# Kernel tuning notes

Hardware: AMD Instinct MI355X
Metric: run time of the kernel (lower is better)

Reference implementation:

```python
import jax, jax.numpy as jnp
import numpy as np

D_MODEL, N_HEADS, D_VALUE = 512, 8, 64
D_HEAD = D_MODEL // N_HEADS


def setup_inputs() -> dict:
    key = jax.random.key(0)
    ks = jax.random.split(key, 5)
    B, T = 2, 2048
    x = jax.random.normal(ks[0], (B, T, D_MODEL), dtype=jnp.float32)
    # torch nn.Linear convention: W has shape [out_features, in_features]
    scale = 0.02
    W_q = jax.random.normal(ks[1], (N_HEADS * D_HEAD, D_MODEL), dtype=jnp.float32) * scale
    W_k = jax.random.normal(ks[2], (N_HEADS * D_HEAD, D_MODEL), dtype=jnp.float32) * scale
    W_v = jax.random.normal(ks[3], (N_HEADS * D_VALUE, D_MODEL), dtype=jnp.float32) * scale
    W_out = jax.random.normal(ks[4], (D_MODEL, N_HEADS * D_VALUE), dtype=jnp.float32) * scale
    return {"x": x, "W_q": W_q, "W_k": W_k, "W_v": W_v, "W_out": W_out}


def _elu_feature_map(t):
    # phi(t) = elu(t) + 1
    return jax.nn.elu(t) + 1.0


def reference(x, W_q, W_k, W_v, W_out):
    B, T, D = x.shape
    H, dh, dv = N_HEADS, D_HEAD, D_VALUE
    # projections (Linear without bias: x @ W.T)
    Q = _elu_feature_map((x @ W_q.T).reshape(B, T, H, dh)).transpose(0, 2, 1, 3)  # [B,H,T,dh]
    K = _elu_feature_map((x @ W_k.T).reshape(B, T, H, dh)).transpose(0, 2, 1, 3)  # [B,H,T,dh]
    V = (x @ W_v.T).reshape(B, T, H, dv).transpose(0, 2, 1, 3)                    # [B,H,T,dv]
    # causal linear attention via cumulative outer-product state
    KV = jnp.einsum('bhti,bhtj->bhtij', K, V)       # [B,H,T,dh,dv]
    S = jnp.cumsum(KV, axis=2)                      # running state
    z = jnp.cumsum(K, axis=2)                       # running normalizer
    num = jnp.einsum('bhti,bhtij->bhtj', Q, S)      # [B,H,T,dv]
    den = jnp.maximum(jnp.einsum('bhti,bhti->bht', Q, z), 1e-6)[..., None]
    out = (num / den).transpose(0, 2, 1, 3).reshape(B, T, H * dv)
    return out @ W_out.T
```

## Files before the change

### kernel.cpp

```cpp
#include <hip/hip_runtime.h>
#include <hip/hip_bf16.h>

#define T_SEQ 2048
#define BATCH 2
#define DMODEL 512
#define NHEAD 8
#define DHEAD 64
#define DVAL 64
#define BH 16
#define CHUNK 64
#define NCHUNK 32
#define MROWS 4096

typedef __bf16 bf16;
typedef __bf16 bf16x8 __attribute__((ext_vector_type(8)));
typedef __bf16 bf16x4 __attribute__((ext_vector_type(4)));
typedef float f32x4 __attribute__((ext_vector_type(4)));

__device__ inline void gload_lds16(const bf16* g, bf16* l) {
  __builtin_amdgcn_global_load_lds((const __attribute__((address_space(1))) void*)g,
                                   (__attribute__((address_space(3))) void*)l, 16, 0, 0);
}

__device__ inline int sw_t(int row, int g) {
  return ((g ^ (row & 7) ^ (row >> 3)) << 3);
}

__global__ __launch_bounds__(256) void k_convert(const float* __restrict__ x,
                          const float* __restrict__ wq,
                          const float* __restrict__ wk,
                          const float* __restrict__ wv,
                          const float* __restrict__ wo,
                          bf16* __restrict__ x_bf,
                          bf16* __restrict__ wqkv_bf,
                          bf16* __restrict__ wo_bf) {
  const int W = DMODEL * DMODEL;
  int i = blockIdx.x * 256 + threadIdx.x;
  {
    f32x4 v = ((const f32x4*)x)[i];
    bf16x4 o; o[0] = (bf16)v[0]; o[1] = (bf16)v[1]; o[2] = (bf16)v[2]; o[3] = (bf16)v[3];
    *(bf16x4*)(x_bf + (size_t)i * 4) = o;
  }
  if (i < W / 4) {
    f32x4 a = ((const f32x4*)wq)[i];
    f32x4 b = ((const f32x4*)wk)[i];
    f32x4 c = ((const f32x4*)wv)[i];
    f32x4 d = ((const f32x4*)wo)[i];
    bf16x4 oa, ob, oc, od;
#pragma unroll
    for (int u = 0; u < 4; u++) { oa[u] = (bf16)a[u]; ob[u] = (bf16)b[u]; oc[u] = (bf16)c[u]; od[u] = (bf16)d[u]; }
    *(bf16x4*)(wqkv_bf + (size_t)i * 4) = oa;
    *(bf16x4*)(wqkv_bf + W + (size_t)i * 4) = ob;
    *(bf16x4*)(wqkv_bf + 2 * W + (size_t)i * 4) = oc;
    *(bf16x4*)(wo_bf + (size_t)i * 4) = od;
  }
}

__global__ __launch_bounds__(256) void k_gemm_qkv(const bf16* __restrict__ A,
                                                  const bf16* __restrict__ B,
                                                  bf16* __restrict__ Q,
                                                  bf16* __restrict__ K,
                                                  bf16* __restrict__ V) {
  __shared__ bf16 sh[12288];
  bf16* As = sh;
  bf16* Bs = sh + 4096;
  const int tid = threadIdx.x;
  const int wvi = tid >> 6, lane = tid & 63;
  const int c = lane & 15, quad = lane >> 4;
  const int m_tile = blockIdx.x * 64, n_tile = blockIdx.y * 128;
  const int r8 = lane >> 3, gp = lane & 7;
  const bf16* Abase = A + (size_t)m_tile * DMODEL;
  const bf16* Bbase = B + (size_t)n_tile * DMODEL;
  const int wn = wvi * 32;

  f32x4 acc[4][2] = {};

  for (int k0 = 0; k0 < DMODEL; k0 += 64) {
    if (k0) __syncthreads();
#pragma unroll
    for (int r = 0; r < 2; r++) {
      int t8 = wvi * 2 + r;
      const bf16* ga = Abase + (size_t)(t8 * 8 + r8) * DMODEL + k0 + ((gp ^ r8) << 3);
      gload_lds16(ga, As + t8 * 8 * 64);
    }
#pragma unroll
    for (int r = 0; r < 4; r++) {
      int t8 = wvi * 4 + r;
      const bf16* gb = Bbase + (size_t)(t8 * 8 + r8) * DMODEL + k0 + ((gp ^ r8) << 3);
      gload_lds16(gb, Bs + t8 * 8 * 64);
    }
    __syncthreads();
#pragma unroll
    for (int ks = 0; ks < 2; ks++) {
      bf16x8 af[4], bfr[2];
#pragma unroll
      for (int i = 0; i < 4; i++)
        af[i] = *(const bf16x8*)(As + (i * 16 + c) * 64 + (((ks * 4 + quad) ^ (c & 7)) << 3));
#pragma unroll
      for (int j = 0; j < 2; j++)
        bfr[j] = *(const bf16x8*)(Bs + (wn + j * 16 + c) * 64 + (((ks * 4 + quad) ^ (c & 7)) << 3));
#pragma unroll
      for (int i = 0; i < 4; i++)
#pragma unroll
        for (int j = 0; j < 2; j++)
          acc[i][j] = __builtin_amdgcn_mfma_f32_16x16x32_bf16(af[i], bfr[j], acc[i][j], 0, 0, 0);
    }
  }

  const bool is_qk = (n_tile < 1024);
  __syncthreads();
#pragma unroll
  for (int i = 0; i < 4; i++)
#pragma unroll
    for (int j = 0; j < 2; j++)
#pragma unroll
      for (int r = 0; r < 4; r++) {
        int row = i * 16 + quad * 4 + r;
        int col = wn + j * 16 + c;
        float v = acc[i][j][r];
        if (is_qk) v = (v > 0.f) ? (v + 1.f) : __expf(v);
        sh[row * 132 + col] = (bf16)v;
      }
  __syncthreads();
  bf16* dst = (n_tile < 512) ? Q : ((n_tile < 1024) ? K : V);
  int nb = n_tile & 511;
#pragma unroll
  for (int q = 0; q < 4; q++) {
    int row = q * 16 + (tid >> 4);
    int col0 = (tid & 15) * 8;
    bf16x8 v8 = *(const bf16x8*)(sh + row * 132 + col0);
    *(bf16x8*)(dst + (size_t)(m_tile + row) * 512 + nb + col0) = v8;
  }
}

__global__ __launch_bounds__(256) void k_gemm_out(const bf16* __restrict__ A,
                                                  const bf16* __restrict__ B,
                                                  float* __restrict__ out) {
  __shared__ bf16 sh[8192];
  bf16* As = sh;
  bf16* Bs = sh + 4096;
  const int tid = threadIdx.x;
  const int wvi = tid >> 6, lane = tid & 63;
  const int c = lane & 15, quad = lane >> 4;
  const int m_tile = blockIdx.x * 64, n_tile = blockIdx.y * 64;
  const int r8 = lane >> 3, gp = lane & 7;
  const bf16* Abase = A + (size_t)m_tile * DMODEL;
  const bf16* Bbase = B + (size_t)n_tile * DMODEL;
  const int wn = wvi * 16;

  f32x4 acc[4] = {};

  for (int k0 = 0; k0 < DMODEL; k0 += 64) {
    if (k0) __syncthreads();
#pragma unroll
    for (int r = 0; r < 2; r++) {
      int t8 = wvi * 2 + r;
      const bf16* ga = Abase + (size_t)(t8 * 8 + r8) * DMODEL + k0 + ((gp ^ r8) << 3);
      gload_lds16(ga, As + t8 * 8 * 64);
    }
#pragma unroll
    for (int r = 0; r < 2; r++) {
      int t8 = wvi * 2 + r;
      const bf16* gb = Bbase + (size_t)(t8 * 8 + r8) * DMODEL + k0 + ((gp ^ r8) << 3);
      gload_lds16(gb, Bs + t8 * 8 * 64);
    }
    __syncthreads();
#pragma unroll
    for (int ks = 0; ks < 2; ks++) {
      bf16x8 af[4], bfr;
#pragma unroll
      for (int i = 0; i < 4; i++)
        af[i] = *(const bf16x8*)(As + (i * 16 + c) * 64 + (((ks * 4 + quad) ^ (c & 7)) << 3));
      bfr = *(const bf16x8*)(Bs + (wn + c) * 64 + (((ks * 4 + quad) ^ (c & 7)) << 3));
#pragma unroll
      for (int i = 0; i < 4; i++)
        acc[i] = __builtin_amdgcn_mfma_f32_16x16x32_bf16(af[i], bfr, acc[i], 0, 0, 0);
    }
  }

  float* shf = (float*)sh;
#pragma unroll
  for (int p = 0; p < 2; p++) {
    __syncthreads();
#pragma unroll
    for (int i2 = 0; i2 < 2; i2++) {
      int i = 2 * p + i2;
#pragma unroll
      for (int r = 0; r < 4; r++)
        shf[(i2 * 16 + quad * 4 + r) * 68 + wn + c] = acc[i][r];
    }
    __syncthreads();
    int row = tid >> 3, col0 = (tid & 7) * 8;
#pragma unroll
    for (int q4 = 0; q4 < 2; q4++) {
      f32x4 v4 = *(const f32x4*)(shf + row * 68 + col0 + q4 * 4);
      *(f32x4*)(out + (size_t)(m_tile + p * 32 + row) * 512 + n_tile + col0 + q4 * 4) = v4;
    }
  }
}

__global__ __launch_bounds__(256) void k_state(const bf16* __restrict__ K,
                                               const bf16* __restrict__ V,
                                               bf16* __restrict__ KVs,
                                               float* __restrict__ zsum) {
  __shared__ bf16 Kt[4096];
  __shared__ bf16 Vt[4096];
  int chunk = blockIdx.x, bh = blockIdx.y;
  int b = bh >> 3, h = bh & 7;
  int tid = threadIdx.x, lane = tid & 63, wvi = tid >> 6;
  int rowbase = b * T_SEQ + chunk * CHUNK;

#pragma unroll
  for (int p = 0; p < 2; p++) {
    int r = p * 32 + (tid >> 3);
    int j0 = (tid & 7) * 8;
    bf16x8 kk  = *(const bf16x8*)(K + (size_t)(rowbase + r) * 512 + h * 64 + j0);
    bf16x8 vvv = *(const bf16x8*)(V + (size_t)(rowbase + r) * 512 + h * 64 + j0);
#pragma unroll
    for (int u = 0; u < 8; u++) {
      int row = j0 + u;
      Kt[row * 64 + sw_t(row, r >> 3) + (r & 7)] = kk[u];
      Vt[row * 64 + sw_t(row, r >> 3) + (r & 7)] = vvv[u];
    }
  }
  __syncthreads();

  int c = lane & 15, quad = lane >> 4;
  f32x4 acc[4] = {};
#pragma unroll
  for (int ks = 0; ks < 2; ks++) {
    int ar = wvi * 16 + c;
    bf16x8 a = *(const bf16x8*)(Vt + ar * 64 + sw_t(ar, ks * 4 + quad));
#pragma unroll
    for (int f = 0; f < 4; f++) {
      int br = f * 16 + c;
      bf16x8 bb = *(const bf16x8*)(Kt + br * 64 + sw_t(br, ks * 4 + quad));
      acc[f] = __builtin_amdgcn_mfma_f32_16x16x32_bf16(a, bb, acc[f], 0, 0, 0);
    }
  }
  bf16* op = KVs + ((size_t)(bh * NCHUNK + chunk) << 12);
  bf16x8 lo, hi;
#pragma unroll
  for (int u = 0; u < 8; u++) {
    lo[u] = (bf16)acc[u >> 2][u & 3];
    hi[u] = (bf16)acc[2 + (u >> 2)][u & 3];
  }
  *(bf16x8*)(op + tid * 16) = lo;
  *(bf16x8*)(op + tid * 16 + 8) = hi;

  if (tid < 64) {
    float s = 0.f;
#pragma unroll
    for (int g = 0; g < 8; g++) {
      bf16x8 kr = *(const bf16x8*)(Kt + tid * 64 + sw_t(tid, g));
#pragma unroll
      for (int u = 0; u < 8; u++) s += (float)kr[u];
    }
    zsum[(size_t)(bh * NCHUNK + chunk) * 64 + tid] = s;
  }
}

__global__ __launch_bounds__(256) void k_attn(const bf16* __restrict__ Q,
                                              const bf16* __restrict__ K,
                                              const bf16* __restrict__ V,
                                              const bf16* __restrict__ KVs,
                                              const float* __restrict__ zsum,
                                              bf16* __restrict__ O) {
  __shared__ bf16 SH[20480];
  bf16* Qs   = SH;
  bf16* Ks   = SH + 4096;
  bf16* Vt   = SH + 8192;
  bf16* Asm  = SH + 12288;
  bf16* Spre = SH + 16384;
  __shared__ float zp4[4][64];
  __shared__ float zpre[64], rsum[64], den[64];

  int chunk = blockIdx.x, bh = blockIdx.y;
  int b = bh >> 3, h = bh & 7;
  int tid = threadIdx.x, lane = tid & 63, wvi = tid >> 6;
  int c = lane & 15, quad = lane >> 4;
  int rowbase = b * T_SEQ + chunk * CHUNK;

#pragma unroll
  for (int p = 0; p < 2; p++) {
    int rbase = p * 32 + wvi * 8;
    int r8 = lane >> 3, gp = lane & 7;
    const bf16* gq = Q + (size_t)(rowbase + rbase + r8) * 512 + h * 64 + ((gp ^ r8) << 3);
    const bf16* gk = K + (size_t)(rowbase + rbase + r8) * 512 + h * 64 + ((gp ^ r8) << 3);
    gload_lds16(gq, Qs + rbase * 64);
    gload_lds16(gk, Ks + rbase * 64);
  }

#pragma unroll
  for (int p = 0; p < 2; p++) {
    int r = p * 32 + (tid >> 3);
    int j0 = (tid & 7) * 8;
    bf16x8 vvv = *(const bf16x8*)(V + (size_t)(rowbase + r) * 512 + h * 64 + j0);
#pragma unroll
    for (int u = 0; u < 8; u++) {
      int row = j0 + u;
      Vt[row * 64 + sw_t(row, r >> 3) + (r & 7)] = vvv[u];
    }
  }

  {
    float accp[16];
#pragma unroll
    for (int u = 0; u < 16; u++) accp[u] = 0.f;
    const bf16* base = KVs + ((size_t)(bh * NCHUNK) << 12) + tid * 16;
    for (int cc = 0; cc < chunk; cc++) {
      const bf16* pp = base + ((size_t)cc << 12);
      bf16x8 a0 = *(const bf16x8*)pp;
      bf16x8 a1 = *(const bf16x8*)(pp + 8);
#pragma unroll
      for (int u = 0; u < 8; u++) { accp[u] += (float)a0[u]; accp[8 + u] += (float)a1[u]; }
    }
#pragma unroll
    for (int s = 0; s < 16; s++) {
      int rowp = wvi * 16 + quad * 4 + (s & 3);
      int colp = (s >> 2) * 16 + c;
      Spre[rowp * 64 + sw_t(rowp, colp >> 3) + (colp & 7)] = (bf16)accp[s];
    }
  }
  {
    int i = tid & 63, qq = tid >> 6;
    float s = 0.f;
    for (int cc = qq; cc < chunk; cc += 4)
      s += zsum[(size_t)(bh * NCHUNK + cc) * 64 + i];
    zp4[qq][i] = s;
  }
  __syncthreads();
  if (tid < 64) zpre[tid] = zp4[0][tid] + zp4[1][tid] + zp4[2][tid] + zp4[3][tid];

  f32x4 sacc[4] = {};
#pragma unroll
  for (int ks = 0; ks < 2; ks++) {
    int ar = 16 * wvi + c;
    bf16x8 a = *(const bf16x8*)(Qs + ar * 64 + (((ks * 4 + quad) ^ (c & 7)) << 3));
#pragma unroll
    for (int j = 0; j < 4; j++) {
      int br = 16 * j + c;
      bf16x8 bb = *(const bf16x8*)(Ks + br * 64 + (((ks * 4 + quad) ^ (c & 7)) << 3));
      sacc[j] = __builtin_amdgcn_mfma_f32_16x16x32_bf16(a, bb, sacc[j], 0, 0, 0);
    }
  }

  float rs[4] = {0.f, 0.f, 0.f, 0.f};
#pragma unroll
  for (int j = 0; j < 4; j++) {
#pragma unroll
    for (int r = 0; r < 4; r++) {
      int t = 16 * wvi + quad * 4 + r, s = 16 * j + c;
      float v = (s <= t) ? sacc[j][r] : 0.f;
      rs[r] += v;
      Asm[t * 64 + sw_t(t, s >> 3) + (s & 7)] = (bf16)v;
    }
  }
#pragma unroll
  for (int r = 0; r < 4; r++) {
    float v = rs[r];
    v += __shfl_xor(v, 1); v += __shfl_xor(v, 2);
    v += __shfl_xor(v, 4); v += __shfl_xor(v, 8);
    if (c == 0) rsum[16 * wvi + quad * 4 + r] = v;
  }
  __syncthreads();

  if (tid < 64) {
    float s = rsum[tid];
    int t7 = tid & 7;
#pragma unroll
    for (int kg = 0; kg < 8; kg++) {
      bf16x8 qv = *(const bf16x8*)(Qs + tid * 64 + ((kg ^ t7) << 3));
#pragma unroll
      for (int u = 0; u < 8; u++) s += (float)qv[u] * zpre[kg * 8 + u];
    }
    den[tid] = fmaxf(s, 1e-6f);
  }

  f32x4 oacc[4] = {};
#pragma unroll
  for (int ks = 0; ks < 2; ks++) {
    int ar = 16 * wvi + c;
    bf16x8 aq = *(const bf16x8*)(Qs + ar * 64 + (((ks * 4 + quad) ^ (c & 7)) << 3));
    bf16x8 aa = *(const bf16x8*)(Asm + ar * 64 + sw_t(ar, ks * 4 + quad));
#pragma unroll
    for (int j = 0; j < 4; j++) {
      int br = 16 * j + c;
      bf16x8 bs = *(const bf16x8*)(Spre + br * 64 + sw_t(br, ks * 4 + quad));
      bf16x8 bv = *(const bf16x8*)(Vt + br * 64 + sw_t(br, ks * 4 + quad));
      oacc[j] = __builtin_amdgcn_mfma_f32_16x16x32_bf16(aq, bs, oacc[j], 0, 0, 0);
      oacc[j] = __builtin_amdgcn_mfma_f32_16x16x32_bf16(aa, bv, oacc[j], 0, 0, 0);
    }
  }
  __syncthreads();

  {
    bf16* shr = SH;
#pragma unroll
    for (int r = 0; r < 4; r++) {
      int t = 16 * wvi + quad * 4 + r;
      float rd = 1.f / den[t];
#pragma unroll
      for (int j = 0; j < 4; j++)
        shr[t * 76 + 16 * j + c] = (bf16)(oacc[j][r] * rd);
    }
    __syncthreads();
    int row = tid >> 2, col0 = (tid & 3) * 16;
    bf16x8 v0 = *(const bf16x8*)(shr + row * 76 + col0);
    bf16x8 v1 = *(const bf16x8*)(shr + row * 76 + col0 + 8);
    bf16* od = O + (size_t)(rowbase + row) * 512 + h * 64 + col0;
    *(bf16x8*)od = v0;
    *(bf16x8*)(od + 8) = v1;
  }
}

extern "C" void kernel_launch(void* const* d_in, const int* in_sizes, int n_in,
                              void* d_out, int out_size, void* d_ws, size_t ws_size,
                              hipStream_t stream) {
  const float* x  = (const float*)d_in[0];
  const float* wq = (const float*)d_in[1];
  const float* wk = (const float*)d_in[2];
  const float* wv = (const float*)d_in[3];
  const float* wo = (const float*)d_in[4];
  float* out = (float*)d_out;

  char* p = (char*)d_ws;
  bf16* x_bf   = (bf16*)p; p += (size_t)MROWS * DMODEL * 2;
  bf16* wqkv_b = (bf16*)p; p += (size_t)3 * DMODEL * DMODEL * 2;
  bf16* wo_b   = (bf16*)p; p += (size_t)DMODEL * DMODEL * 2;
  bf16* Qb     = (bf16*)p; p += (size_t)MROWS * 512 * 2;
  bf16* Kb     = (bf16*)p; p += (size_t)MROWS * 512 * 2;
  bf16* Vb     = (bf16*)p; p += (size_t)MROWS * 512 * 2;
  bf16* Ob     = (bf16*)p; p += (size_t)MROWS * 512 * 2;
  bf16* KVs    = (bf16*)p; p += (size_t)BH * NCHUNK * DHEAD * DVAL * 2;
  float* zs    = (float*)p; p += (size_t)BH * NCHUNK * DHEAD * 4;

  k_convert<<<2048, 256, 0, stream>>>(x, wq, wk, wv, wo, x_bf, wqkv_b, wo_b);
  k_gemm_qkv<<<dim3(MROWS / 64, (3 * DMODEL) / 128), 256, 0, stream>>>(
      x_bf, wqkv_b, Qb, Kb, Vb);
  k_state<<<dim3(NCHUNK, BH), 256, 0, stream>>>(Kb, Vb, KVs, zs);
  k_attn<<<dim3(NCHUNK, BH), 256, 0, stream>>>(Qb, Kb, Vb, KVs, zs, Ob);
  k_gemm_out<<<dim3(MROWS / 64, DMODEL / 64), 256, 0, stream>>>(Ob, wo_b, out);
}
```

Before: 109.9 us.

## Fuse all five stages into one cooperative persistent kernel with grid syncs

Replaces the five separate launches (convert, QKV GEMM, chunk state, attention, output GEMM) with a single cooperative kernel of 768 blocks that separates the stages with grid.sync(). The aim is to remove per-launch overhead and the gaps between kernels on a small problem. In exchange, the grid is capped at 768 resident blocks, later stages leave some blocks idle, and grid-wide barriers have their own cost. Occupancy depends on three blocks fitting per CU with a 42KB shared buffer.

```diff
diff --git a/kernel.cpp b/kernel.cpp
--- a/kernel.cpp
+++ b/kernel.cpp
@@ -1,5 +1,8 @@
 #include <hip/hip_runtime.h>
 #include <hip/hip_bf16.h>
+#include <hip/hip_cooperative_groups.h>
+
+namespace cg = cooperative_groups;
 
 #define T_SEQ 2048
 #define BATCH 2
@@ -12,6 +15,8 @@
 #define NCHUNK 32
 #define MROWS 4096
 
+#define GRID_BLOCKS 768
+
 typedef __bf16 bf16;
 typedef __bf16 bf16x8 __attribute__((ext_vector_type(8)));
 typedef __bf16 bf16x4 __attribute__((ext_vector_type(4)));
@@ -26,391 +31,389 @@
   return ((g ^ (row & 7) ^ (row >> 3)) << 3);
 }
 
-__global__ __launch_bounds__(256) void k_convert(const float* __restrict__ x,
-                          const float* __restrict__ wq,
-                          const float* __restrict__ wk,
-                          const float* __restrict__ wv,
-                          const float* __restrict__ wo,
-                          bf16* __restrict__ x_bf,
-                          bf16* __restrict__ wqkv_bf,
-                          bf16* __restrict__ wo_bf) {
-  const int W = DMODEL * DMODEL;
-  int i = blockIdx.x * 256 + threadIdx.x;
-  {
-    f32x4 v = ((const f32x4*)x)[i];
-    bf16x4 o; o[0] = (bf16)v[0]; o[1] = (bf16)v[1]; o[2] = (bf16)v[2]; o[3] = (bf16)v[3];
-    *(bf16x4*)(x_bf + (size_t)i * 4) = o;
-  }
-  if (i < W / 4) {
-    f32x4 a = ((const f32x4*)wq)[i];
-    f32x4 b = ((const f32x4*)wk)[i];
-    f32x4 c = ((const f32x4*)wv)[i];
-    f32x4 d = ((const f32x4*)wo)[i];
-    bf16x4 oa, ob, oc, od;
-#pragma unroll
-    for (int u = 0; u < 4; u++) { oa[u] = (bf16)a[u]; ob[u] = (bf16)b[u]; oc[u] = (bf16)c[u]; od[u] = (bf16)d[u]; }
-    *(bf16x4*)(wqkv_bf + (size_t)i * 4) = oa;
-    *(bf16x4*)(wqkv_bf + W + (size_t)i * 4) = ob;
-    *(bf16x4*)(wqkv_bf + 2 * W + (size_t)i * 4) = oc;
-    *(bf16x4*)(wo_bf + (size_t)i * 4) = od;
-  }
-}
-
-__global__ __launch_bounds__(256) void k_gemm_qkv(const bf16* __restrict__ A,
-                                                  const bf16* __restrict__ B,
-                                                  bf16* __restrict__ Q,
-                                                  bf16* __restrict__ K,
-                                                  bf16* __restrict__ V) {
-  __shared__ bf16 sh[12288];
-  bf16* As = sh;
-  bf16* Bs = sh + 4096;
+__global__ __launch_bounds__(256, 3) void k_fused(
+    const float* __restrict__ x,
+    const float* __restrict__ wq,
+    const float* __restrict__ wk,
+    const float* __restrict__ wv,
+    const float* __restrict__ wo,
+    bf16* __restrict__ x_bf,
+    bf16* __restrict__ wqkv_bf,
+    bf16* __restrict__ wo_bf,
+    bf16* __restrict__ Qb,
+    bf16* __restrict__ Kb,
+    bf16* __restrict__ Vb,
+    bf16* __restrict__ Ob,
+    bf16* __restrict__ KVs,
+    float* __restrict__ zsum,
+    float* __restrict__ out) {
+  __shared__ __align__(16) char SHB[43008];
+  bf16* sh = (bf16*)SHB;
+
   const int tid = threadIdx.x;
+  const int bid = blockIdx.x;
+  cg::grid_group grid = cg::this_grid();
+
   const int wvi = tid >> 6, lane = tid & 63;
   const int c = lane & 15, quad = lane >> 4;
-  const int m_tile = blockIdx.x * 64, n_tile = blockIdx.y * 128;
   const int r8 = lane >> 3, gp = lane & 7;
-  const bf16* Abase = A + (size_t)m_tile * DMODEL;
-  const bf16* Bbase = B + (size_t)n_tile * DMODEL;
-  const int wn = wvi * 32;
-
-  f32x4 acc[4][2] = {};
-
-  for (int k0 = 0; k0 < DMODEL; k0 += 64) {
-    if (k0) __syncthreads();
-#pragma unroll
-    for (int r = 0; r < 2; r++) {
-      int t8 = wvi * 2 + r;
-      const bf16* ga = Abase + (size_t)(t8 * 8 + r8) * DMODEL + k0 + ((gp ^ r8) << 3);
-      gload_lds16(ga, As + t8 * 8 * 64);
+
+  {
+    const int W = DMODEL * DMODEL;
+    for (int i = bid * 256 + tid; i < (MROWS * DMODEL) / 4; i += GRID_BLOCKS * 256) {
+      f32x4 v = ((const f32x4*)x)[i];
+      bf16x4 o; o[0] = (bf16)v[0]; o[1] = (bf16)v[1]; o[2] = (bf16)v[2]; o[3] = (bf16)v[3];
+      *(bf16x4*)(x_bf + (size_t)i * 4) = o;
+      if (i < W / 4) {
+        f32x4 a = ((const f32x4*)wq)[i];
+        f32x4 b = ((const f32x4*)wk)[i];
+        f32x4 cc = ((const f32x4*)wv)[i];
+        f32x4 d = ((const f32x4*)wo)[i];
+        bf16x4 oa, ob, oc, od;
+#pragma unroll
+        for (int u = 0; u < 4; u++) { oa[u] = (bf16)a[u]; ob[u] = (bf16)b[u]; oc[u] = (bf16)cc[u]; od[u] = (bf16)d[u]; }
+        *(bf16x4*)(wqkv_bf + (size_t)i * 4) = oa;
+        *(bf16x4*)(wqkv_bf + W + (size_t)i * 4) = ob;
+        *(bf16x4*)(wqkv_bf + 2 * W + (size_t)i * 4) = oc;
+        *(bf16x4*)(wo_bf + (size_t)i * 4) = od;
+      }
+    }
+  }
+  grid.sync();
+
+  {
+    bf16* As = sh;
+    bf16* Bs = sh + 4096;
+    const int bx = bid & 63, by = bid >> 6;
+    const int m_tile = bx * 64, n_tile = by * 128;
+    const bf16* Abase = x_bf + (size_t)m_tile * DMODEL;
+    const bf16* Bbase = wqkv_bf + (size_t)n_tile * DMODEL;
+    const int wn = wvi * 32;
+
+    f32x4 acc[4][2] = {};
+
+    for (int k0 = 0; k0 < DMODEL; k0 += 64) {
+      if (k0) __syncthreads();
+#pragma unroll
+      for (int r = 0; r < 2; r++) {
+        int t8 = wvi * 2 + r;
+        const bf16* ga = Abase + (size_t)(t8 * 8 + r8) * DMODEL + k0 + ((gp ^ r8) << 3);
+        gload_lds16(ga, As + t8 * 8 * 64);
+      }
+#pragma unroll
+      for (int r = 0; r < 4; r++) {
+        int t8 = wvi * 4 + r;
+        const bf16* gb = Bbase + (size_t)(t8 * 8 + r8) * DMODEL + k0 + ((gp ^ r8) << 3);
+        gload_lds16(gb, Bs + t8 * 8 * 64);
+      }
+      __syncthreads();
+#pragma unroll
+      for (int ks = 0; ks < 2; ks++) {
+        bf16x8 af[4], bfr[2];
+#pragma unroll
+        for (int i = 0; i < 4; i++)
+          af[i] = *(const bf16x8*)(As + (i * 16 + c) * 64 + (((ks * 4 + quad) ^ (c & 7)) << 3));
+#pragma unroll
+        for (int j = 0; j < 2; j++)
+          bfr[j] = *(const bf16x8*)(Bs + (wn + j * 16 + c) * 64 + (((ks * 4 + quad) ^ (c & 7)) << 3));
+#pragma unroll
+        for (int i = 0; i < 4; i++)
+#pragma unroll
+          for (int j = 0; j < 2; j++)
+            acc[i][j] = __builtin_amdgcn_mfma_f32_16x16x32_bf16(af[i], bfr[j], acc[i][j], 0, 0, 0);
+      }
+    }
+
+    const bool is_qk = (n_tile < 1024);
+    __syncthreads();
+#pragma unroll
+    for (int i = 0; i < 4; i++)
+#pragma unroll
+      for (int j = 0; j < 2; j++)
+#pragma unroll
+        for (int r = 0; r < 4; r++) {
+          int row = i * 16 + quad * 4 + r;
+          int col = wn + j * 16 + c;
+          float v = acc[i][j][r];
+          if (is_qk) v = (v > 0.f) ? (v + 1.f) : __expf(v);
+          sh[row * 132 + col] = (bf16)v;
+        }
+    __syncthreads();
+    bf16* dst = (n_tile < 512) ? Qb : ((n_tile < 1024) ? Kb : Vb);
+    int nb = n_tile & 511;
+#pragma unroll
+    for (int q = 0; q < 4; q++) {
+      int row = q * 16 + (tid >> 4);
+      int col0 = (tid & 15) * 8;
+      bf16x8 v8 = *(const bf16x8*)(sh + row * 132 + col0);
+      *(bf16x8*)(dst + (size_t)(m_tile + row) * 512 + nb + col0) = v8;
+    }
+  }
+  grid.sync();
+
+  if (bid < NCHUNK * BH) {
+    bf16* Kt = sh;
+    bf16* Vt = sh + 4096;
+    int chunk = bid & 31, bh = bid >> 5;
+    int b = bh >> 3, h = bh & 7;
+    int rowbase = b * T_SEQ + chunk * CHUNK;
+
+#pragma unroll
+    for (int p = 0; p < 2; p++) {
+      int r = p * 32 + (tid >> 3);
+      int j0 = (tid & 7) * 8;
+      bf16x8 kk  = *(const bf16x8*)(Kb + (size_t)(rowbase + r) * 512 + h * 64 + j0);
+      bf16x8 vvv = *(const bf16x8*)(Vb + (size_t)(rowbase + r) * 512 + h * 64 + j0);
+#pragma unroll
+      for (int u = 0; u < 8; u++) {
+        int row = j0 + u;
+        Kt[row * 64 + sw_t(row, r >> 3) + (r & 7)] = kk[u];
+        Vt[row * 64 + sw_t(row, r >> 3) + (r & 7)] = vvv[u];
+      }
+    }
+    __syncthreads();
+
+    f32x4 acc[4] = {};
+#pragma unroll
+    for (int ks = 0; ks < 2; ks++) {
+      int ar = wvi * 16 + c;
+      bf16x8 a = *(const bf16x8*)(Vt + ar * 64 + sw_t(ar, ks * 4 + quad));
+#pragma unroll
+      for (int f = 0; f < 4; f++) {
+        int br = f * 16 + c;
+        bf16x8 bb = *(const bf16x8*)(Kt + br * 64 + sw_t(br, ks * 4 + quad));
+        acc[f] = __builtin_amdgcn_mfma_f32_16x16x32_bf16(a, bb, acc[f], 0, 0, 0);
+      }
+    }
+    bf16* op = KVs + ((size_t)(bh * NCHUNK + chunk) << 12);
+    bf16x8 lo, hi;
+#pragma unroll
+    for (int u = 0; u < 8; u++) {
+      lo[u] = (bf16)acc[u >> 2][u & 3];
+      hi[u] = (bf16)acc[2 + (u >> 2)][u & 3];
+    }
+    *(bf16x8*)(op + tid * 16) = lo;
+    *(bf16x8*)(op + tid * 16 + 8) = hi;
+
+    if (tid < 64) {
+      float s = 0.f;
+#pragma unroll
+      for (int g = 0; g < 8; g++) {
+        bf16x8 kr = *(const bf16x8*)(Kt + tid * 64 + sw_t(tid, g));
+#pragma unroll
+        for (int u = 0; u < 8; u++) s += (float)kr[u];
+      }
+      zsum[(size_t)(bh * NCHUNK + chunk) * 64 + tid] = s;
+    }
+  }
+  grid.sync();
+
+  if (bid < NCHUNK * BH) {
+    bf16* Qs   = sh;
+    bf16* Ks   = sh + 4096;
+    bf16* Vt   = sh + 8192;
+    bf16* Asm  = sh + 12288;
+    bf16* Spre = sh + 16384;
+    float* zp4  = (float*)(SHB + 40960);
+    float* zpre = (float*)(SHB + 40960 + 1024);
+    float* rsum = zpre + 64;
+    float* den  = rsum + 64;
+
+    int chunk = bid & 31, bh = bid >> 5;
+    int b = bh >> 3, h = bh & 7;
+    int rowbase = b * T_SEQ + chunk * CHUNK;
+
+#pragma unroll
+    for (int p = 0; p < 2; p++) {
+      int rbase = p * 32 + wvi * 8;
+      const bf16* gq = Qb + (size_t)(rowbase + rbase + r8) * 512 + h * 64 + ((gp ^ r8) << 3);
+      const bf16* gk = Kb + (size_t)(rowbase + rbase + r8) * 512 + h * 64 + ((gp ^ r8) << 3);
+      gload_lds16(gq, Qs + rbase * 64);
+      gload_lds16(gk, Ks + rbase * 64);
+    }
+
+#pragma unroll
+    for (int p = 0; p < 2; p++) {
+      int r = p * 32 + (tid >> 3);
+      int j0 = (tid & 7) * 8;
+      bf16x8 vvv = *(const bf16x8*)(Vb + (size_t)(rowbase + r) * 512 + h * 64 + j0);
+#pragma unroll
+      for (int u = 0; u < 8; u++) {
+        int row = j0 + u;
+        Vt[row * 64 + sw_t(row, r >> 3) + (r & 7)] = vvv[u];
+      }
+    }
+
+    {
+      float accp[16];
+#pragma unroll
+      for (int u = 0; u < 16; u++) accp[u] = 0.f;
+      const bf16* base = KVs + ((size_t)(bh * NCHUNK) << 12) + tid * 16;
+      for (int cc = 0; cc < chunk; cc++) {
+        const bf16* pp = base + ((size_t)cc << 12);
+        bf16x8 a0 = *(const bf16x8*)pp;
+        bf16x8 a1 = *(const bf16x8*)(pp + 8);
+#pragma unroll
+        for (int u = 0; u < 8; u++) { accp[u] += (float)a0[u]; accp[8 + u] += (float)a1[u]; }
+      }
+#pragma unroll
+      for (int s = 0; s < 16; s++) {
+        int rowp = wvi * 16 + quad * 4 + (s & 3);
+        int colp = (s >> 2) * 16 + c;
+        Spre[rowp * 64 + sw_t(rowp, colp >> 3) + (colp & 7)] = (bf16)accp[s];
+      }
+    }
+    {
+      int i = tid & 63, qq = tid >> 6;
+      float s = 0.f;
+      for (int cc = qq; cc < chunk; cc += 4)
+        s += zsum[(size_t)(bh * NCHUNK + cc) * 64 + i];
+      zp4[qq * 64 + i] = s;
+    }
+    __syncthreads();
+    if (tid < 64) zpre[tid] = zp4[0 * 64 + tid] + zp4[1 * 64 + tid] + zp4[2 * 64 + tid] + zp4[3 * 64 + tid];
+
+    f32x4 sacc[4] = {};
+#pragma unroll
+    for (int ks = 0; ks < 2; ks++) {
+      int ar = 16 * wvi + c;
+      bf16x8 a = *(const bf16x8*)(Qs + ar * 64 + (((ks * 4 + quad) ^ (c & 7)) << 3));
+#pragma unroll
+      for (int j = 0; j < 4; j++) {
+        int br = 16 * j + c;
+        bf16x8 bb = *(const bf16x8*)(Ks + br * 64 + (((ks * 4 + quad) ^ (c & 7)) << 3));
+        sacc[j] = __builtin_amdgcn_mfma_f32_16x16x32_bf16(a, bb, sacc[j], 0, 0, 0);
+      }
+    }
+
+    float rs[4] = {0.f, 0.f, 0.f, 0.f};
+#pragma unroll
+    for (int j = 0; j < 4; j++) {
+#pragma unroll
+      for (int r = 0; r < 4; r++) {
+        int t = 16 * wvi + quad * 4 + r, s = 16 * j + c;
+        float v = (s <= t) ? sacc[j][r] : 0.f;
+        rs[r] += v;
+        Asm[t * 64 + sw_t(t, s >> 3) + (s & 7)] = (bf16)v;
+      }
     }
 #pragma unroll
     for (int r = 0; r < 4; r++) {
-      int t8 = wvi * 4 + r;
-      const bf16* gb = Bbase + (size_t)(t8 * 8 + r8) * DMODEL + k0 + ((gp ^ r8) << 3);
-      gload_lds16(gb, Bs + t8 * 8 * 64);
-    }
-    __syncthreads();
+      float v = rs[r];
+      v += __shfl_xor(v, 1); v += __shfl_xor(v, 2);
+      v += __shfl_xor(v, 4); v += __shfl_xor(v, 8);
+      if (c == 0) rsum[16 * wvi + quad * 4 + r] = v;
+    }
+    __syncthreads();
+
+    if (tid < 64) {
+      float s = rsum[tid];
+      int t7 = tid & 7;
+#pragma unroll
+      for (int kg = 0; kg < 8; kg++) {
+        bf16x8 qv = *(const bf16x8*)(Qs + tid * 64 + ((kg ^ t7) << 3));
+#pragma unroll
+        for (int u = 0; u < 8; u++) s += (float)qv[u] * zpre[kg * 8 + u];
+      }
+      den[tid] = fmaxf(s, 1e-6f);
+    }
+
+    f32x4 oacc[4] = {};
 #pragma unroll
     for (int ks = 0; ks < 2; ks++) {
-      bf16x8 af[4], bfr[2];
-#pragma unroll
-      for (int i = 0; i < 4; i++)
-        af[i] = *(const bf16x8*)(As + (i * 16 + c) * 64 + (((ks * 4 + quad) ^ (c & 7)) << 3));
-#pragma unroll
-      for (int j = 0; j < 2; j++)
-        bfr[j] = *(const bf16x8*)(Bs + (wn + j * 16 + c) * 64 + (((ks * 4 + quad) ^ (c & 7)) << 3));
-#pragma unroll
-      for (int i = 0; i < 4; i++)
-#pragma unroll
-        for (int j = 0; j < 2; j++)
-          acc[i][j] = __builtin_amdgcn_mfma_f32_16x16x32_bf16(af[i], bfr[j], acc[i][j], 0, 0, 0);
+      int ar = 16 * wvi + c;
+      bf16x8 aq = *(const bf16x8*)(Qs + ar * 64 + (((ks * 4 + quad) ^ (c & 7)) << 3));
+      bf16x8 aa = *(const bf16x8*)(Asm + ar * 64 + sw_t(ar, ks * 4 + quad));
+#pragma unroll
+      for (int j = 0; j < 4; j++) {
+        int br = 16 * j + c;
+        bf16x8 bs = *(const bf16x8*)(Spre + br * 64 + sw_t(br, ks * 4 + quad));
+        bf16x8 bv = *(const bf16x8*)(Vt + br * 64 + sw_t(br, ks * 4 + quad));
+        oacc[j] = __builtin_amdgcn_mfma_f32_16x16x32_bf16(aq, bs, oacc[j], 0, 0, 0);
+        oacc[j] = __builtin_amdgcn_mfma_f32_16x16x32_bf16(aa, bv, oacc[j], 0, 0, 0);
+      }
+    }
+    __syncthreads();
+
+    {
+      bf16* shr = sh;
+#pragma unroll
+      for (int r = 0; r < 4; r++) {
+        int t = 16 * wvi + quad * 4 + r;
+        float rd = 1.f / den[t];
+#pragma unroll
+        for (int j = 0; j < 4; j++)
+          shr[t * 76 + 16 * j + c] = (bf16)(oacc[j][r] * rd);
+      }
+      __syncthreads();
+      int row = tid >> 2, col0 = (tid & 3) * 16;
+      bf16x8 v0 = *(const bf16x8*)(shr + row * 76 + col0);
+      bf16x8 v1 = *(const bf16x8*)(shr + row * 76 + col0 + 8);
+      bf16* od = Ob + (size_t)(rowbase + row) * 512 + h * 64 + col0;
+      *(bf16x8*)od = v0;
+      *(bf16x8*)(od + 8) = v1;
     }
   }
-
-  const bool is_qk = (n_tile < 1024);
-  __syncthreads();
-#pragma unroll
-  for (int i = 0; i < 4; i++)
-#pragma unroll
-    for (int j = 0; j < 2; j++)
-#pragma unroll
-      for (int r = 0; r < 4; r++) {
-        int row = i * 16 + quad * 4 + r;
-        int col = wn + j * 16 + c;
-        float v = acc[i][j][r];
-        if (is_qk) v = (v > 0.f) ? (v + 1.f) : __expf(v);
-        sh[row * 132 + col] = (bf16)v;
-      }
-  __syncthreads();
-  bf16* dst = (n_tile < 512) ? Q : ((n_tile < 1024) ? K : V);
-  int nb = n_tile & 511;
-#pragma unroll
-  for (int q = 0; q < 4; q++) {
-    int row = q * 16 + (tid >> 4);
-    int col0 = (tid & 15) * 8;
-    bf16x8 v8 = *(const bf16x8*)(sh + row * 132 + col0);
-    *(bf16x8*)(dst + (size_t)(m_tile + row) * 512 + nb + col0) = v8;
-  }
-}
-
-__global__ __launch_bounds__(256) void k_gemm_out(const bf16* __restrict__ A,
-                                                  const bf16* __restrict__ B,
-                                                  float* __restrict__ out) {
-  __shared__ bf16 sh[8192];
-  bf16* As = sh;
-  bf16* Bs = sh + 4096;
-  const int tid = threadIdx.x;
-  const int wvi = tid >> 6, lane = tid & 63;
-  const int c = lane & 15, quad = lane >> 4;
-  const int m_tile = blockIdx.x * 64, n_tile = blockIdx.y * 64;
-  const int r8 = lane >> 3, gp = lane & 7;
-  const bf16* Abase = A + (size_t)m_tile * DMODEL;
-  const bf16* Bbase = B + (size_t)n_tile * DMODEL;
-  const int wn = wvi * 16;
-
-  f32x4 acc[4] = {};
-
-  for (int k0 = 0; k0 < DMODEL; k0 += 64) {
-    if (k0) __syncthreads();
-#pragma unroll
-    for (int r = 0; r < 2; r++) {
-      int t8 = wvi * 2 + r;
-      const bf16* ga = Abase + (size_t)(t8 * 8 + r8) * DMODEL + k0 + ((gp ^ r8) << 3);
-      gload_lds16(ga, As + t8 * 8 * 64);
-    }
-#pragma unroll
-    for (int r = 0; r < 2; r++) {
-      int t8 = wvi * 2 + r;
-      const bf16* gb = Bbase + (size_t)(t8 * 8 + r8) * DMODEL + k0 + ((gp ^ r8) << 3);
-      gload_lds16(gb, Bs + t8 * 8 * 64);
-    }
-    __syncthreads();
-#pragma unroll
-    for (int ks = 0; ks < 2; ks++) {
-      bf16x8 af[4], bfr;
-#pragma unroll
-      for (int i = 0; i < 4; i++)
-        af[i] = *(const bf16x8*)(As + (i * 16 + c) * 64 + (((ks * 4 + quad) ^ (c & 7)) << 3));
-      bfr = *(const bf16x8*)(Bs + (wn + c) * 64 + (((ks * 4 + quad) ^ (c & 7)) << 3));
-#pragma unroll
-      for (int i = 0; i < 4; i++)
-        acc[i] = __builtin_amdgcn_mfma_f32_16x16x32_bf16(af[i], bfr, acc[i], 0, 0, 0);
-    }
-  }
-
-  float* shf = (float*)sh;
-#pragma unroll
-  for (int p = 0; p < 2; p++) {
-    __syncthreads();
-#pragma unroll
-    for (int i2 = 0; i2 < 2; i2++) {
-      int i = 2 * p + i2;
-#pragma unroll
-      for (int r = 0; r < 4; r++)
-        shf[(i2 * 16 + quad * 4 + r) * 68 + wn + c] = acc[i][r];
-    }
-    __syncthreads();
-    int row = tid >> 3, col0 = (tid & 7) * 8;
-#pragma unroll
-    for (int q4 = 0; q4 < 2; q4++) {
-      f32x4 v4 = *(const f32x4*)(shf + row * 68 + col0 + q4 * 4);
-      *(f32x4*)(out + (size_t)(m_tile + p * 32 + row) * 512 + n_tile + col0 + q4 * 4) = v4;
-    }
-  }
-}
-
-__global__ __launch_bounds__(256) void k_state(const bf16* __restrict__ K,
-                                               const bf16* __restrict__ V,
-                                               bf16* __restrict__ KVs,
-                                               float* __restrict__ zsum) {
-  __shared__ bf16 Kt[4096];
-  __shared__ bf16 Vt[4096];
-  int chunk = blockIdx.x, bh = blockIdx.y;
-  int b = bh >> 3, h = bh & 7;
-  int tid = threadIdx.x, lane = tid & 63, wvi = tid >> 6;
-  int rowbase = b * T_SEQ + chunk * CHUNK;
-
-#pragma unroll
-  for (int p = 0; p < 2; p++) {
-    int r = p * 32 + (tid >> 3);
-    int j0 = (tid & 7) * 8;
-    bf16x8 kk  = *(const bf16x8*)(K + (size_t)(rowbase + r) * 512 + h * 64 + j0);
-    bf16x8 vvv = *(const bf16x8*)(V + (size_t)(rowbase + r) * 512 + h * 64 + j0);
-#pragma unroll
-    for (int u = 0; u < 8; u++) {
-      int row = j0 + u;
-      Kt[row * 64 + sw_t(row, r >> 3) + (r & 7)] = kk[u];
-      Vt[row * 64 + sw_t(row, r >> 3) + (r & 7)] = vvv[u];
-    }
-  }
-  __syncthreads();
-
-  int c = lane & 15, quad = lane >> 4;
-  f32x4 acc[4] = {};
-#pragma unroll
-  for (int ks = 0; ks < 2; ks++) {
-    int ar = wvi * 16 + c;
-    bf16x8 a = *(const bf16x8*)(Vt + ar * 64 + sw_t(ar, ks * 4 + quad));
-#pragma unroll
-    for (int f = 0; f < 4; f++) {
-      int br = f * 16 + c;
-      bf16x8 bb = *(const bf16x8*)(Kt + br * 64 + sw_t(br, ks * 4 + quad));
-      acc[f] = __builtin_amdgcn_mfma_f32_16x16x32_bf16(a, bb, acc[f], 0, 0, 0);
-    }
-  }
-  bf16* op = KVs + ((size_t)(bh * NCHUNK + chunk) << 12);
-  bf16x8 lo, hi;
-#pragma unroll
-  for (int u = 0; u < 8; u++) {
-    lo[u] = (bf16)acc[u >> 2][u & 3];
-    hi[u] = (bf16)acc[2 + (u >> 2)][u & 3];
-  }
-  *(bf16x8*)(op + tid * 16) = lo;
-  *(bf16x8*)(op + tid * 16 + 8) = hi;
-
-  if (tid < 64) {
-    float s = 0.f;
-#pragma unroll
-    for (int g = 0; g < 8; g++) {
-      bf16x8 kr = *(const bf16x8*)(Kt + tid * 64 + sw_t(tid, g));
-#pragma unroll
-      for (int u = 0; u < 8; u++) s += (float)kr[u];
-    }
-    zsum[(size_t)(bh * NCHUNK + chunk) * 64 + tid] = s;
-  }
-}
-
-__global__ __launch_bounds__(256) void k_attn(const bf16* __restrict__ Q,
-                                              const bf16* __restrict__ K,
-                                              const bf16* __restrict__ V,
-                                              const bf16* __restrict__ KVs,
-                                              const float* __restrict__ zsum,
-                                              bf16* __restrict__ O) {
-  __shared__ bf16 SH[20480];
-  bf16* Qs   = SH;
-  bf16* Ks   = SH + 4096;
-  bf16* Vt   = SH + 8192;
-  bf16* Asm  = SH + 12288;
-  bf16* Spre = SH + 16384;
-  __shared__ float zp4[4][64];
-  __shared__ float zpre[64], rsum[64], den[64];
-
-  int chunk = blockIdx.x, bh = blockIdx.y;
-  int b = bh >> 3, h = bh & 7;
-  int tid = threadIdx.x, lane = tid & 63, wvi = tid >> 6;
-  int c = lane & 15, quad = lane >> 4;
-  int rowbase = b * T_SEQ + chunk * CHUNK;
-
-#pragma unroll
-  for (int p = 0; p < 2; p++) {
-    int rbase = p * 32 + wvi * 8;
-    int r8 = lane >> 3, gp = lane & 7;
-    const bf16* gq = Q + (size_t)(rowbase + rbase + r8) * 512 + h * 64 + ((gp ^ r8) << 3);
-    const bf16* gk = K + (size_t)(rowbase + rbase + r8) * 512 + h * 64 + ((gp ^ r8) << 3);
-    gload_lds16(gq, Qs + rbase * 64);
-    gload_lds16(gk, Ks + rbase * 64);
-  }
-
-#pragma unroll
-  for (int p = 0; p < 2; p++) {
-    int r = p * 32 + (tid >> 3);
-    int j0 = (tid & 7) * 8;
-    bf16x8 vvv = *(const bf16x8*)(V + (size_t)(rowbase + r) * 512 + h * 64 + j0);
-#pragma unroll
-    for (int u = 0; u < 8; u++) {
-      int row = j0 + u;
-      Vt[row * 64 + sw_t(row, r >> 3) + (r & 7)] = vvv[u];
-    }
-  }
-
-  {
-    float accp[16];
-#pragma unroll
-    for (int u = 0; u < 16; u++) accp[u] = 0.f;
-    const bf16* base = KVs + ((size_t)(bh * NCHUNK) << 12) + tid * 16;
-    for (int cc = 0; cc < chunk; cc++) {
-      const bf16* pp = base + ((size_t)cc << 12);
-      bf16x8 a0 = *(const bf16x8*)pp;
-      bf16x8 a1 = *(const bf16x8*)(pp + 8);
-#pragma unroll
-      for (int u = 0; u < 8; u++) { accp[u] += (float)a0[u]; accp[8 + u] += (float)a1[u]; }
-    }
-#pragma unroll
-    for (int s = 0; s < 16; s++) {
-      int rowp = wvi * 16 + quad * 4 + (s & 3);
-      int colp = (s >> 2) * 16 + c;
-      Spre[rowp * 64 + sw_t(rowp, colp >> 3) + (colp & 7)] = (bf16)accp[s];
-    }
-  }
-  {
-    int i = tid & 63, qq = tid >> 6;
-    float s = 0.f;
-    for (int cc = qq; cc < chunk; cc += 4)
-      s += zsum[(size_t)(bh * NCHUNK + cc) * 64 + i];
-    zp4[qq][i] = s;
-  }
-  __syncthreads();
-  if (tid < 64) zpre[tid] = zp4[0][tid] + zp4[1][tid] + zp4[2][tid] + zp4[3][tid];
-
-  f32x4 sacc[4] = {};
-#pragma unroll
-  for (int ks = 0; ks < 2; ks++) {
-    int ar = 16 * wvi + c;
-    bf16x8 a = *(const bf16x8*)(Qs + ar * 64 + (((ks * 4 + quad) ^ (c & 7)) << 3));
-#pragma unroll
-    for (int j = 0; j < 4; j++) {
-      int br = 16 * j + c;
-      bf16x8 bb = *(const bf16x8*)(Ks + br * 64 + (((ks * 4 + quad) ^ (c & 7)) << 3));
-      sacc[j] = __builtin_amdgcn_mfma_f32_16x16x32_bf16(a, bb, sacc[j], 0, 0, 0);
-    }
-  }
-
-  float rs[4] = {0.f, 0.f, 0.f, 0.f};
-#pragma unroll
-  for (int j = 0; j < 4; j++) {
-#pragma unroll
-    for (int r = 0; r < 4; r++) {
-      int t = 16 * wvi + quad * 4 + r, s = 16 * j + c;
-      float v = (s <= t) ? sacc[j][r] : 0.f;
-      rs[r] += v;
-      Asm[t * 64 + sw_t(t, s >> 3) + (s & 7)] = (bf16)v;
-    }
-  }
-#pragma unroll
-  for (int r = 0; r < 4; r++) {
-    float v = rs[r];
-    v += __shfl_xor(v, 1); v += __shfl_xor(v, 2);
-    v += __shfl_xor(v, 4); v += __shfl_xor(v, 8);
-    if (c == 0) rsum[16 * wvi + quad * 4 + r] = v;
-  }
-  __syncthreads();
-
-  if (tid < 64) {
-    float s = rsum[tid];
-    int t7 = tid & 7;
-#pragma unroll
-    for (int kg = 0; kg < 8; kg++) {
-      bf16x8 qv = *(const bf16x8*)(Qs + tid * 64 + ((kg ^ t7) << 3));
-#pragma unroll
-      for (int u = 0; u < 8; u++) s += (float)qv[u] * zpre[kg * 8 + u];
-    }
-    den[tid] = fmaxf(s, 1e-6f);
-  }
-
-  f32x4 oacc[4] = {};
-#pragma unroll
-  for (int ks = 0; ks < 2; ks++) {
-    int ar = 16 * wvi + c;
-    bf16x8 aq = *(const bf16x8*)(Qs + ar * 64 + (((ks * 4 + quad) ^ (c & 7)) << 3));
-    bf16x8 aa = *(const bf16x8*)(Asm + ar * 64 + sw_t(ar, ks * 4 + quad));
-#pragma unroll
-    for (int j = 0; j < 4; j++) {
-      int br = 16 * j + c;
-      bf16x8 bs = *(const bf16x8*)(Spre + br * 64 + sw_t(br, ks * 4 + quad));
-      bf16x8 bv = *(const bf16x8*)(Vt + br * 64 + sw_t(br, ks * 4 + quad));
-      oacc[j] = __builtin_amdgcn_mfma_f32_16x16x32_bf16(aq, bs, oacc[j], 0, 0, 0);
-      oacc[j] = __builtin_amdgcn_mfma_f32_16x16x32_bf16(aa, bv, oacc[j], 0, 0, 0);
-    }
-  }
-  __syncthreads();
-
-  {
-    bf16* shr = SH;
-#pragma unroll
-    for (int r = 0; r < 4; r++) {
-      int t = 16 * wvi + quad * 4 + r;
-      float rd = 1.f / den[t];
-#pragma unroll
-      for (int j = 0; j < 4; j++)
-        shr[t * 76 + 16 * j + c] = (bf16)(oacc[j][r] * rd);
-    }
-    __syncthreads();
-    int row = tid >> 2, col0 = (tid & 3) * 16;
-    bf16x8 v0 = *(const bf16x8*)(shr + row * 76 + col0);
-    bf16x8 v1 = *(const bf16x8*)(shr + row * 76 + col0 + 8);
-    bf16* od = O + (size_t)(rowbase + row) * 512 + h * 64 + col0;
-    *(bf16x8*)od = v0;
-    *(bf16x8*)(od + 8) = v1;
+  grid.sync();
+
+  if (bid < 512) {
+    bf16* As = sh;
+    bf16* Bs = sh + 4096;
+    const int bx = bid & 63, by = bid >> 6;
+    const int m_tile = bx * 64, n_tile = by * 64;
+    const bf16* Abase = Ob + (size_t)m_tile * DMODEL;
+    const bf16* Bbase = wo_bf + (size_t)n_tile * DMODEL;
+    const int wn = wvi * 16;
+
+    f32x4 acc[4] = {};
+
+    for (int k0 = 0; k0 < DMODEL; k0 += 64) {
+      if (k0) __syncthreads();
+#pragma unroll
+      for (int r = 0; r < 2; r++) {
+        int t8 = wvi * 2 + r;
+        const bf16* ga = Abase + (size_t)(t8 * 8 + r8) * DMODEL + k0 + ((gp ^ r8) << 3);
+        gload_lds16(ga, As + t8 * 8 * 64);
+      }
+#pragma unroll
+      for (int r = 0; r < 2; r++) {
+        int t8 = wvi * 2 + r;
+        const bf16* gb = Bbase + (size_t)(t8 * 8 + r8) * DMODEL + k0 + ((gp ^ r8) << 3);
+        gload_lds16(gb, Bs + t8 * 8 * 64);
+      }
+      __syncthreads();
+#pragma unroll
+      for (int ks = 0; ks < 2; ks++) {
+        bf16x8 af[4], bfr;
+#pragma unroll
+        for (int i = 0; i < 4; i++)
+          af[i] = *(const bf16x8*)(As + (i * 16 + c) * 64 + (((ks * 4 + quad) ^ (c & 7)) << 3));
+        bfr = *(const bf16x8*)(Bs + (wn + c) * 64 + (((ks * 4 + quad) ^ (c & 7)) << 3));
+#pragma unroll
+        for (int i = 0; i < 4; i++)
+          acc[i] = __builtin_amdgcn_mfma_f32_16x16x32_bf16(af[i], bfr, acc[i], 0, 0, 0);
+      }
+    }
+
+    float* shf = (float*)SHB;
+#pragma unroll
+    for (int p = 0; p < 2; p++) {
+      __syncthreads();
+#pragma unroll
+      for (int i2 = 0; i2 < 2; i2++) {
+        int i = 2 * p + i2;
+#pragma unroll
+        for (int r = 0; r < 4; r++)
+          shf[(i2 * 16 + quad * 4 + r) * 68 + wn + c] = acc[i][r];
+      }
+      __syncthreads();
+      int row = tid >> 3, col0 = (tid & 7) * 8;
+#pragma unroll
+      for (int q4 = 0; q4 < 2; q4++) {
+        f32x4 v4 = *(const f32x4*)(shf + row * 68 + col0 + q4 * 4);
+        *(f32x4*)(out + (size_t)(m_tile + p * 32 + row) * 512 + n_tile + col0 + q4 * 4) = v4;
+      }
+    }
   }
 }
 
@@ -435,10 +438,9 @@
   bf16* KVs    = (bf16*)p; p += (size_t)BH * NCHUNK * DHEAD * DVAL * 2;
   float* zs    = (float*)p; p += (size_t)BH * NCHUNK * DHEAD * 4;
 
-  k_convert<<<2048, 256, 0, stream>>>(x, wq, wk, wv, wo, x_bf, wqkv_b, wo_b);
-  k_gemm_qkv<<<dim3(MROWS / 64, (3 * DMODEL) / 128), 256, 0, stream>>>(
-      x_bf, wqkv_b, Qb, Kb, Vb);
-  k_state<<<dim3(NCHUNK, BH), 256, 0, stream>>>(Kb, Vb, KVs, zs);
-  k_attn<<<dim3(NCHUNK, BH), 256, 0, stream>>>(Qb, Kb, Vb, KVs, zs, Ob);
-  k_gemm_out<<<dim3(MROWS / 64, DMODEL / 64), 256, 0, stream>>>(Ob, wo_b, out);
+  void* args[] = {(void*)&x, (void*)&wq, (void*)&wk, (void*)&wv, (void*)&wo,
+                  (void*)&x_bf, (void*)&wqkv_b, (void*)&wo_b,
+                  (void*)&Qb, (void*)&Kb, (void*)&Vb, (void*)&Ob,
+                  (void*)&KVs, (void*)&zs, (void*)&out};
+  hipLaunchCooperativeKernel((void*)k_fused, dim3(GRID_BLOCKS), dim3(256), args, 0, stream);
 }
```

Measured after the change: 431.1 us. +292.3%, slower.

## Add separate exclusive prefix-scan kernel for chunk KV states

Applied to the files above, without the earlier changes.

Adds a k_scan kernel that computes an exclusive prefix sum of the per-chunk KV states into an fp32 buffer, one block per batch-head. k_attn then loads its prefix state directly instead of summing all earlier chunks. This removes the quadratic redundant reduction across chunks, where later chunks read up to 31 states. The cost is an extra kernel launch, a serial 32-step scan running on only 16 blocks, and a larger fp32 intermediate buffer.

```diff
diff --git a/kernel.cpp b/kernel.cpp
--- a/kernel.cpp
+++ b/kernel.cpp
@@ -260,10 +260,35 @@
   }
 }
 
+__global__ __launch_bounds__(256) void k_scan(const bf16* __restrict__ KVs,
+                                              float* __restrict__ CumS) {
+  int bh = blockIdx.x;
+  int tid = threadIdx.x;
+  const bf16* base = KVs + ((size_t)(bh * NCHUNK) << 12) + tid * 16;
+  float* obase = CumS + ((size_t)(bh * NCHUNK) << 12) + tid * 16;
+  float acc[16];
+#pragma unroll
+  for (int u = 0; u < 16; u++) acc[u] = 0.f;
+#pragma unroll 2
+  for (int cc = 0; cc < NCHUNK; cc++) {
+    float* o = obase + ((size_t)cc << 12);
+#pragma unroll
+    for (int q = 0; q < 4; q++) {
+      f32x4 v; v[0] = acc[q * 4]; v[1] = acc[q * 4 + 1]; v[2] = acc[q * 4 + 2]; v[3] = acc[q * 4 + 3];
+      *(f32x4*)(o + q * 4) = v;
+    }
+    const bf16* pp = base + ((size_t)cc << 12);
+    bf16x8 a0 = *(const bf16x8*)pp;
+    bf16x8 a1 = *(const bf16x8*)(pp + 8);
+#pragma unroll
+    for (int u = 0; u < 8; u++) { acc[u] += (float)a0[u]; acc[8 + u] += (float)a1[u]; }
+  }
+}
+
 __global__ __launch_bounds__(256) void k_attn(const bf16* __restrict__ Q,
                                               const bf16* __restrict__ K,
                                               const bf16* __restrict__ V,
-                                              const bf16* __restrict__ KVs,
+                                              const float* __restrict__ CumS,
                                               const float* __restrict__ zsum,
                                               bf16* __restrict__ O) {
   __shared__ bf16 SH[20480];
@@ -291,6 +316,12 @@
     gload_lds16(gk, Ks + rbase * 64);
   }
 
+  const float* cbase = CumS + ((size_t)(bh * NCHUNK + chunk) << 12) + tid * 16;
+  f32x4 p0 = *(const f32x4*)(cbase);
+  f32x4 p1 = *(const f32x4*)(cbase + 4);
+  f32x4 p2 = *(const f32x4*)(cbase + 8);
+  f32x4 p3 = *(const f32x4*)(cbase + 12);
+
 #pragma unroll
   for (int p = 0; p < 2; p++) {
     int r = p * 32 + (tid >> 3);
@@ -306,15 +337,7 @@
   {
     float accp[16];
 #pragma unroll
-    for (int u = 0; u < 16; u++) accp[u] = 0.f;
-    const bf16* base = KVs + ((size_t)(bh * NCHUNK) << 12) + tid * 16;
-    for (int cc = 0; cc < chunk; cc++) {
-      const bf16* pp = base + ((size_t)cc << 12);
-      bf16x8 a0 = *(const bf16x8*)pp;
-      bf16x8 a1 = *(const bf16x8*)(pp + 8);
-#pragma unroll
-      for (int u = 0; u < 8; u++) { accp[u] += (float)a0[u]; accp[8 + u] += (float)a1[u]; }
-    }
+    for (int u = 0; u < 4; u++) { accp[u] = p0[u]; accp[4 + u] = p1[u]; accp[8 + u] = p2[u]; accp[12 + u] = p3[u]; }
 #pragma unroll
     for (int s = 0; s < 16; s++) {
       int rowp = wvi * 16 + quad * 4 + (s & 3);
@@ -434,11 +457,13 @@
   bf16* Ob     = (bf16*)p; p += (size_t)MROWS * 512 * 2;
   bf16* KVs    = (bf16*)p; p += (size_t)BH * NCHUNK * DHEAD * DVAL * 2;
   float* zs    = (float*)p; p += (size_t)BH * NCHUNK * DHEAD * 4;
+  float* CumS  = (float*)p; p += (size_t)BH * NCHUNK * DHEAD * DVAL * 4;
 
   k_convert<<<2048, 256, 0, stream>>>(x, wq, wk, wv, wo, x_bf, wqkv_b, wo_b);
   k_gemm_qkv<<<dim3(MROWS / 64, (3 * DMODEL) / 128), 256, 0, stream>>>(
       x_bf, wqkv_b, Qb, Kb, Vb);
   k_state<<<dim3(NCHUNK, BH), 256, 0, stream>>>(Kb, Vb, KVs, zs);
-  k_attn<<<dim3(NCHUNK, BH), 256, 0, stream>>>(Qb, Kb, Vb, KVs, zs, Ob);
+  k_scan<<<dim3(BH), 256, 0, stream>>>(KVs, CumS);
+  k_attn<<<dim3(NCHUNK, BH), 256, 0, stream>>>(Qb, Kb, Vb, CumS, zs, Ob);
   k_gemm_out<<<dim3(MROWS / 64, DMODEL / 64), 256, 0, stream>>>(Ob, wo_b, out);
 }
```

Result: slower. 124.8 us (+13.6%).
